# Optimization experiments

Measured on AMD Instinct MI355X. Metric: run time of the kernel, lower is better.

Reference implementation:

```python
import jax, jax.numpy as jnp
import numpy as np

F, K, V, ITERS = 150000, 5, 100000, 5
S = 2 ** K  # factor state space
MLP_SIZE = 2 * ITERS * S + ITERS * 2  # 330
NEG = -1e30
SHIFT = -500.0

# static bit table: bits[state, slot] in {0,1}
_BITS = ((np.arange(S)[:, None] >> np.arange(K)[None, :]) & 1).astype(np.int32)  # [S,K]
_BITS_T = jnp.asarray(_BITS.T)  # [K,S]
# mask bias for grouped logsumexp: bias[slot, b, state] = 0 if bits[state,slot]==b else NEG
_BIAS = jnp.asarray(np.where(_BITS.T[:, None, :] == np.arange(2)[None, :, None], 0.0, NEG).astype(np.float32))  # [K,2,S]


def neg_inf_to_zero(x):
    return jnp.where(jnp.isneginf(x), 0.0, x)


def expand(msg):
    # msg [F,K,2] -> [F,K,S]: broadcast each slot message over factor states by that slot's bit
    return msg[:, jnp.arange(K)[:, None], _BITS_T]


def setup_inputs() -> dict:
    key = jax.random.key(0)
    k0, k1 = jax.random.split(key)
    factor_potentials = jax.random.normal(k0, (F, S), dtype=jnp.float32)
    var_idx = jax.random.randint(k1, (F, K), 0, V, dtype=jnp.int32)
    prv_v2f = jnp.zeros((F, K, 2), jnp.float32)
    prv_f2v = jnp.zeros((F, K, 2), jnp.float32)
    prv_fb = jax.nn.log_softmax(factor_potentials, axis=1)
    # bethe MLP initialized exactly as in the torch module
    lin1_w = jnp.eye(MLP_SIZE, dtype=jnp.float32)
    lin1_b = jnp.zeros((MLP_SIZE,), jnp.float32)
    num_ones = 2 * S + 2
    lin2_w = jnp.zeros((1, MLP_SIZE), jnp.float32).at[0, -num_ones:].set(1.0)
    lin2_b = jnp.zeros((1,), jnp.float32)
    return {"factor_potentials": factor_potentials, "var_idx": var_idx,
            "prv_v2f": prv_v2f, "prv_f2v": prv_f2v, "prv_fb": prv_fb,
            "lin1_w": lin1_w, "lin1_b": lin1_b, "lin2_w": lin2_w, "lin2_b": lin2_b}


def _shifted_relu(x):
    return jnp.maximum(x, SHIFT)


def reference(factor_potentials, var_idx, prv_v2f, prv_f2v, prv_fb, lin1_w, lin1_b, lin2_w, lin2_b):
    var_flat = var_idx.reshape(-1)
    deg = jax.ops.segment_sum(jnp.ones((F * K,), jnp.float32), var_flat, num_segments=V)  # var_degrees
    pooled_states = []
    fb, v2f = prv_fb, prv_v2f
    for _ in range(ITERS):
        # factor->var messages, no double counting: subtract the slot's own incoming message
        scores = fb[:, None, :] - expand(v2f)                    # [F,K,S]
        m = jax.nn.logsumexp(scores[:, :, None, :] + _BIAS[None], axis=-1)  # [F,K,2]
        m = jax.nn.log_softmax(m, axis=-1)
        # var beliefs: gather all incoming factor->var messages
        vb = jax.ops.segment_sum(m.reshape(-1, 2), var_flat, num_segments=V)  # [V,2]
        vb = jax.nn.log_softmax(vb, axis=-1)
        # var->factor messages, no double counting
        v2f = jax.nn.log_softmax(vb[var_idx] - m, axis=-1)        # [F,K,2]
        # factor beliefs
        fb = factor_potentials + expand(v2f).sum(axis=1)          # [F,S]
        fb = fb - jax.nn.logsumexp(fb, axis=1, keepdims=True)
        # pooled Bethe free-energy features for this iteration
        e_fb = jnp.exp(fb)
        energy = jnp.sum(e_fb * neg_inf_to_zero(factor_potentials), axis=0)     # [S]
        fac_ent = -jnp.sum(e_fb * neg_inf_to_zero(fb), axis=0)                  # [S]
        var_term = jnp.sum((deg - 1.0)[:, None] * jnp.exp(vb) * neg_inf_to_zero(vb), axis=0)  # [2]
        pooled_states.append(jnp.concatenate([energy, fac_ent, var_term])[None, :])  # [1, 2S+2]
    x = jnp.concatenate(pooled_states, axis=1)   # [1, MLP_SIZE]
    h = _shifted_relu(x @ lin1_w.T + lin1_b)
    out = _shifted_relu(h @ lin2_w.T + lin2_b)   # [1,1] estimated ln(Z)
    return out
```

## Files before the change

kernel.cpp:

```cpp
#include <hip/hip_runtime.h>

#define F_N   150000
#define K_N   5
#define S_N   32
#define V_N   100000
#define NITER 5
#define MLP_N 330
#define SHIFTV (-500.0f)
#define W_ELL 32

#define FBLK  ((F_N + 255) / 256)
#define GBLK  ((V_N * 8 + 255) / 256)
#define EBLK  ((F_N * K_N + 255) / 256)

__device__ __forceinline__ float lse2(float a, float b) {
    float mx = fmaxf(a, b);
    return mx + __logf(__expf(a - mx) + __expf(b - mx));
}

__global__ __launch_bounds__(256) void k_build(
    const float* __restrict__ prv_fb,
    const float* __restrict__ prv_v2f,
    const int*   __restrict__ vidx,
    float2*      __restrict__ m2,
    int*         __restrict__ deg,
    int*         __restrict__ entries)
{
    int e = blockIdx.x * 256 + threadIdx.x;
    if (e >= F_N * K_N) return;
    int f = e / K_N;
    int k = e - f * K_N;
    int v = vidx[e];

    int pos = atomicAdd(&deg[v], 1);

    float fb[S_N];
    const float4* p4 = reinterpret_cast<const float4*>(prv_fb + (size_t)f * S_N);
    #pragma unroll
    for (int i = 0; i < S_N / 4; ++i) {
        float4 q = p4[i];
        fb[i*4+0] = q.x; fb[i*4+1] = q.y; fb[i*4+2] = q.z; fb[i*4+3] = q.w;
    }
    float M = fb[0];
    #pragma unroll
    for (int s = 1; s < S_N; ++s) M = fmaxf(M, fb[s]);
    float T = 0.0f, S0 = 0.0f;
    #pragma unroll
    for (int s = 0; s < S_N; ++s) {
        float t = __expf(fb[s] - M);
        T += t;
        if (((s >> k) & 1) == 0) S0 += t;
    }
    float v0 = prv_v2f[(size_t)e * 2 + 0];
    float v1 = prv_v2f[(size_t)e * 2 + 1];
    float u0 = __logf(S0)     - v0;
    float u1 = __logf(T - S0) - v1;
    float l  = lse2(u0, u1);
    m2[k*F_N + f] = make_float2(u0 - l, u1 - l);

    int slot = (pos < W_ELL) ? v * W_ELL + pos : V_N * W_ELL;
    entries[slot] = k * F_N + f;
}

__global__ __launch_bounds__(256) void k_gather(
    const float2* __restrict__ m2,
    const int*    __restrict__ deg,
    const int*    __restrict__ entries,
    float2*       __restrict__ vb,
    float2*       __restrict__ cpart,
    int iter)
{
    __shared__ float2 wred[4];
    int t = blockIdx.x * 256 + threadIdx.x;
    int v = t >> 3, sub = t & 7;
    int lane = threadIdx.x & 63;

    float a0 = 0.0f, a1 = 0.0f;
    int n = 0;
    if (v < V_N) {
        n = deg[v];
        int nn = n < W_ELL ? n : W_ELL;
        const int* row = entries + (size_t)v * W_ELL;
        for (int i = sub; i < nn; i += 8) {
            float2 mm = m2[row[i]];
            a0 += mm.x; a1 += mm.y;
        }
    }
    a0 += __shfl_xor(a0, 1); a1 += __shfl_xor(a1, 1);
    a0 += __shfl_xor(a0, 2); a1 += __shfl_xor(a1, 2);
    a0 += __shfl_xor(a0, 4); a1 += __shfl_xor(a1, 4);

    float c0 = 0.0f, c1 = 0.0f;
    if (v < V_N && sub == 0) {
        vb[v] = make_float2(a0, a1);
        float l = lse2(a0, a1);
        float b0 = a0 - l, b1 = a1 - l;
        float dm1 = (float)n - 1.0f;
        c0 = dm1 * __expf(b0) * b0;
        c1 = dm1 * __expf(b1) * b1;
    }
    #pragma unroll
    for (int mk = 32; mk >= 1; mk >>= 1) {
        c0 += __shfl_xor(c0, mk);
        c1 += __shfl_xor(c1, mk);
    }
    if (lane == 0) wred[threadIdx.x >> 6] = make_float2(c0, c1);
    __syncthreads();
    if (threadIdx.x == 0) {
        float2 s = wred[0];
        s.x += wred[1].x + wred[2].x + wred[3].x;
        s.y += wred[1].y + wred[2].y + wred[3].y;
        cpart[iter * GBLK + blockIdx.x] = s;
    }
}

template <bool LAST>
__global__ __launch_bounds__(256) void k_iter(
    const float*  __restrict__ pot,
    const int*    __restrict__ vidx,
    float2*       __restrict__ m2,
    const float2* __restrict__ vb,
    float*        __restrict__ fpart,
    int iter)
{
    const int lane = threadIdx.x & 63;
    __shared__ float red[256];

    int f = blockIdx.x * 256 + threadIdx.x;
    bool valid = f < F_N;
    int fc = valid ? f : (F_N - 1);

    float2 mm[K_N];
    #pragma unroll
    for (int k = 0; k < K_N; ++k) mm[k] = m2[k*F_N + fc];
    int vi[K_N];
    #pragma unroll
    for (int k = 0; k < K_N; ++k) vi[k] = vidx[(size_t)fc * K_N + k];

    float v2f[K_N][2];
    #pragma unroll
    for (int k = 0; k < K_N; ++k) {
        float2 b = vb[vi[k]];
        float a0 = b.x - mm[k].x;
        float a1 = b.y - mm[k].y;
        float l = lse2(a0, a1);
        v2f[k][0] = a0 - l;
        v2f[k][1] = a1 - l;
    }

    float fb[S_N];
    const float4* p4 = reinterpret_cast<const float4*>(pot + (size_t)fc * S_N);
    #pragma unroll
    for (int i = 0; i < S_N / 4; ++i) {
        float4 pv = p4[i];
        int s = i * 4;
        fb[s+0] = pv.x + v2f[0][(s+0)&1] + v2f[1][((s+0)>>1)&1] + v2f[2][((s+0)>>2)&1] + v2f[3][((s+0)>>3)&1] + v2f[4][((s+0)>>4)&1];
        fb[s+1] = pv.y + v2f[0][(s+1)&1] + v2f[1][((s+1)>>1)&1] + v2f[2][((s+1)>>2)&1] + v2f[3][((s+1)>>3)&1] + v2f[4][((s+1)>>4)&1];
        fb[s+2] = pv.z + v2f[0][(s+2)&1] + v2f[1][((s+2)>>1)&1] + v2f[2][((s+2)>>2)&1] + v2f[3][((s+2)>>3)&1] + v2f[4][((s+2)>>4)&1];
        fb[s+3] = pv.w + v2f[0][(s+3)&1] + v2f[1][((s+3)>>1)&1] + v2f[2][((s+3)>>2)&1] + v2f[3][((s+3)>>3)&1] + v2f[4][((s+3)>>4)&1];
    }

    float M = fb[0];
    #pragma unroll
    for (int s = 1; s < S_N; ++s) M = fmaxf(M, fb[s]);

    float T = 0.0f;
    float S0[K_N] = {0.f, 0.f, 0.f, 0.f, 0.f};
    #pragma unroll
    for (int s = 0; s < S_N; ++s) {
        float t = __expf(fb[s] - M);
        T += t;
        #pragma unroll
        for (int k = 0; k < K_N; ++k)
            if (((s >> k) & 1) == 0) S0[k] += t;
    }

    if (!LAST) {
        #pragma unroll
        for (int k = 0; k < K_N; ++k) {
            float u0 = __logf(S0[k])     - v2f[k][0];
            float u1 = __logf(T - S0[k]) - v2f[k][1];
            float l  = lse2(u0, u1);
            if (valid) m2[k*F_N + f] = make_float2(u0 - l, u1 - l);
        }
    }

    float invT = 1.0f / T;
    float logT = __logf(T);
    float arr[2 * S_N];
    #pragma unroll
    for (int s = 0; s < S_N; ++s) {
        float p   = __expf(fb[s] - M) * invT;
        float fbn = fb[s] - M - logT;
        float w   = v2f[0][s&1] + v2f[1][(s>>1)&1] + v2f[2][(s>>2)&1]
                  + v2f[3][(s>>3)&1] + v2f[4][(s>>4)&1];
        float po  = fb[s] - w;
        arr[s]       = valid ? p * po   : 0.0f;
        arr[S_N + s] = valid ? -p * fbn : 0.0f;
    }

    #pragma unroll
    for (int mk = 32; mk >= 1; mk >>= 1) {
        bool upper = (lane & mk) != 0;
        #pragma unroll
        for (int j = 0; j < mk; ++j) {
            float send = upper ? arr[j] : arr[j + mk];
            float recv = __shfl_xor(send, mk);
            float keep = upper ? arr[j + mk] : arr[j];
            arr[j] = keep + recv;
        }
    }

    red[threadIdx.x] = arr[0];
    __syncthreads();
    if (threadIdx.x < 64) {
        float s = red[threadIdx.x] + red[64 + threadIdx.x]
                + red[128 + threadIdx.x] + red[192 + threadIdx.x];
        fpart[((size_t)iter * FBLK + blockIdx.x) * 64 + threadIdx.x] = s;
    }
}

__global__ __launch_bounds__(256) void k_vt(
    const float*  __restrict__ fpart,
    const float2* __restrict__ cpart,
    float*        __restrict__ x)
{
    __shared__ float red[256];
    int b = blockIdx.x, t = threadIdx.x;
    float acc = 0.0f;
    if (b < 320) {
        int it = b >> 6, s = b & 63;
        for (int i = t; i < FBLK; i += 256)
            acc += fpart[((size_t)it * FBLK + i) * 64 + s];
    } else {
        int idx = b - 320;
        int it = idx >> 1, c = idx & 1;
        for (int i = t; i < GBLK; i += 256) {
            float2 p = cpart[it * GBLK + i];
            acc += c ? p.y : p.x;
        }
    }
    red[t] = acc;
    __syncthreads();
    #pragma unroll
    for (int off = 128; off >= 1; off >>= 1) {
        if (t < off) red[t] += red[t + off];
        __syncthreads();
    }
    if (t == 0) {
        if (b < 320) {
            int it = b >> 6, s = b & 63;
            x[it*66 + s] = red[0];
        } else {
            int idx = b - 320;
            int it = idx >> 1, c = idx & 1;
            x[it*66 + 64 + c] = red[0];
        }
    }
}

__global__ __launch_bounds__(64) void k_mlp1(
    const float* __restrict__ x, const float* __restrict__ w1,
    const float* __restrict__ b1, float* __restrict__ h)
{
    int j = blockIdx.x;
    int lane = threadIdx.x;
    float s = 0.0f;
    for (int i = lane; i < MLP_N; i += 64) s += x[i] * w1[(size_t)j * MLP_N + i];
    #pragma unroll
    for (int mk = 32; mk >= 1; mk >>= 1) s += __shfl_xor(s, mk);
    if (lane == 0) h[j] = fmaxf(s + b1[j], SHIFTV);
}

__global__ __launch_bounds__(64) void k_mlp2(
    const float* __restrict__ h, const float* __restrict__ w2,
    const float* __restrict__ b2, float* __restrict__ out)
{
    int lane = threadIdx.x;
    float s = 0.0f;
    for (int i = lane; i < MLP_N; i += 64) s += h[i] * w2[i];
    #pragma unroll
    for (int mk = 32; mk >= 1; mk >>= 1) s += __shfl_xor(s, mk);
    if (lane == 0) out[0] = fmaxf(s + b2[0], SHIFTV);
}

extern "C" void kernel_launch(void* const* d_in, const int* in_sizes, int n_in,
                              void* d_out, int out_size, void* d_ws, size_t ws_size,
                              hipStream_t stream)
{
    (void)in_sizes; (void)n_in; (void)out_size; (void)ws_size;
    const float* pot  = (const float*)d_in[0];
    const int*   vidx = (const int*)  d_in[1];
    const float* pv2f = (const float*)d_in[2];
    const float* pfb  = (const float*)d_in[4];
    const float* w1   = (const float*)d_in[5];
    const float* b1   = (const float*)d_in[6];
    const float* w2   = (const float*)d_in[7];
    const float* b2   = (const float*)d_in[8];

    float2* m2      = (float2*)d_ws;
    float2* vb      = m2 + 5 * F_N;
    float2* cpart   = vb + V_N;
    float*  fpart   = (float*)(cpart + NITER * GBLK);
    float*  x       = fpart + (size_t)NITER * FBLK * 64;
    float*  h       = x + MLP_N;
    int*    entries = (int*)(h + MLP_N);
    int*    deg     = entries + (size_t)V_N * W_ELL + 64;

    hipMemsetAsync(deg, 0, (size_t)V_N * sizeof(int), stream);

    k_build<<<EBLK, 256, 0, stream>>>(pfb, pv2f, vidx, m2, deg, entries);

    for (int it = 0; it < NITER; ++it) {
        k_gather<<<GBLK, 256, 0, stream>>>(m2, deg, entries, vb, cpart, it);
        if (it < NITER - 1)
            k_iter<false><<<FBLK, 256, 0, stream>>>(pot, vidx, m2, vb, fpart, it);
        else
            k_iter<true><<<FBLK, 256, 0, stream>>>(pot, vidx, m2, vb, fpart, it);
    }

    k_vt<<<330, 256, 0, stream>>>(fpart, cpart, x);
    k_mlp1<<<MLP_N, 64, 0, stream>>>(x, w1, b1, h);
    k_mlp2<<<1, 64, 0, stream>>>(h, w2, b2, (float*)d_out);
}
```

Before: 203.7 us.

## Split each factor across two threads in the factor iteration kernel

```diff
diff --git a/kernel.cpp b/kernel.cpp
--- a/kernel.cpp
+++ b/kernel.cpp
@@ -10,6 +10,7 @@
 #define W_ELL 32
 
 #define FBLK  ((F_N + 255) / 256)
+#define F2BLK ((2*F_N + 255) / 256)
 #define GBLK  ((V_N * 8 + 255) / 256)
 #define EBLK  ((F_N * K_N + 255) / 256)
 
@@ -124,99 +125,120 @@
     int iter)
 {
     const int lane = threadIdx.x & 63;
-    __shared__ float red[256];
-
-    int f = blockIdx.x * 256 + threadIdx.x;
+    __shared__ float red[4][64];
+
+    int t = blockIdx.x * 256 + threadIdx.x;
+    int f = t >> 1, p = t & 1;
     bool valid = f < F_N;
     int fc = valid ? f : (F_N - 1);
 
-    float2 mm[K_N];
-    #pragma unroll
-    for (int k = 0; k < K_N; ++k) mm[k] = m2[k*F_N + fc];
-    int vi[K_N];
-    #pragma unroll
-    for (int k = 0; k < K_N; ++k) vi[k] = vidx[(size_t)fc * K_N + k];
-
-    float v2f[K_N][2];
+    float v2f[K_N][2] = {{0,0},{0,0},{0,0},{0,0},{0,0}};
     #pragma unroll
     for (int k = 0; k < K_N; ++k) {
-        float2 b = vb[vi[k]];
-        float a0 = b.x - mm[k].x;
-        float a1 = b.y - mm[k].y;
-        float l = lse2(a0, a1);
-        v2f[k][0] = a0 - l;
-        v2f[k][1] = a1 - l;
-    }
-
-    float fb[S_N];
-    const float4* p4 = reinterpret_cast<const float4*>(pot + (size_t)fc * S_N);
-    #pragma unroll
-    for (int i = 0; i < S_N / 4; ++i) {
+        bool mine = p ? (k >= 3) : (k < 3);
+        if (mine) {
+            int vi = vidx[(size_t)fc * K_N + k];
+            float2 mmk = m2[k*F_N + fc];
+            float2 b = vb[vi];
+            float a0 = b.x - mmk.x;
+            float a1 = b.y - mmk.y;
+            float l = lse2(a0, a1);
+            v2f[k][0] = a0 - l;
+            v2f[k][1] = a1 - l;
+        }
+    }
+    #pragma unroll
+    for (int k = 0; k < K_N; ++k) {
+        bool mine = p ? (k >= 3) : (k < 3);
+        float o0 = __shfl_xor(v2f[k][0], 1);
+        float o1 = __shfl_xor(v2f[k][1], 1);
+        if (!mine) { v2f[k][0] = o0; v2f[k][1] = o1; }
+    }
+
+    float fb[16];
+    const float4* p4 = reinterpret_cast<const float4*>(pot + (size_t)fc * S_N + p * 16);
+    #pragma unroll
+    for (int i = 0; i < 4; ++i) {
         float4 pv = p4[i];
-        int s = i * 4;
-        fb[s+0] = pv.x + v2f[0][(s+0)&1] + v2f[1][((s+0)>>1)&1] + v2f[2][((s+0)>>2)&1] + v2f[3][((s+0)>>3)&1] + v2f[4][((s+0)>>4)&1];
-        fb[s+1] = pv.y + v2f[0][(s+1)&1] + v2f[1][((s+1)>>1)&1] + v2f[2][((s+1)>>2)&1] + v2f[3][((s+1)>>3)&1] + v2f[4][((s+1)>>4)&1];
-        fb[s+2] = pv.z + v2f[0][(s+2)&1] + v2f[1][((s+2)>>1)&1] + v2f[2][((s+2)>>2)&1] + v2f[3][((s+2)>>3)&1] + v2f[4][((s+2)>>4)&1];
-        fb[s+3] = pv.w + v2f[0][(s+3)&1] + v2f[1][((s+3)>>1)&1] + v2f[2][((s+3)>>2)&1] + v2f[3][((s+3)>>3)&1] + v2f[4][((s+3)>>4)&1];
+        int s = p*16 + i*4;
+        fb[i*4+0] = pv.x + v2f[0][(s+0)&1] + v2f[1][((s+0)>>1)&1] + v2f[2][((s+0)>>2)&1] + v2f[3][((s+0)>>3)&1] + v2f[4][((s+0)>>4)&1];
+        fb[i*4+1] = pv.y + v2f[0][(s+1)&1] + v2f[1][((s+1)>>1)&1] + v2f[2][((s+1)>>2)&1] + v2f[3][((s+1)>>3)&1] + v2f[4][((s+1)>>4)&1];
+        fb[i*4+2] = pv.z + v2f[0][(s+2)&1] + v2f[1][((s+2)>>1)&1] + v2f[2][((s+2)>>2)&1] + v2f[3][((s+2)>>3)&1] + v2f[4][((s+2)>>4)&1];
+        fb[i*4+3] = pv.w + v2f[0][(s+3)&1] + v2f[1][((s+3)>>1)&1] + v2f[2][((s+3)>>2)&1] + v2f[3][((s+3)>>3)&1] + v2f[4][((s+3)>>4)&1];
     }
 
     float M = fb[0];
     #pragma unroll
-    for (int s = 1; s < S_N; ++s) M = fmaxf(M, fb[s]);
+    for (int j = 1; j < 16; ++j) M = fmaxf(M, fb[j]);
+    M = fmaxf(M, __shfl_xor(M, 1));
 
     float T = 0.0f;
     float S0[K_N] = {0.f, 0.f, 0.f, 0.f, 0.f};
     #pragma unroll
-    for (int s = 0; s < S_N; ++s) {
-        float t = __expf(fb[s] - M);
-        T += t;
+    for (int j = 0; j < 16; ++j) {
+        int s = p*16 + j;
+        float e = __expf(fb[j] - M);
+        T += e;
         #pragma unroll
         for (int k = 0; k < K_N; ++k)
-            if (((s >> k) & 1) == 0) S0[k] += t;
-    }
+            if (((s >> k) & 1) == 0) S0[k] += e;
+    }
+    T += __shfl_xor(T, 1);
+    #pragma unroll
+    for (int k = 0; k < K_N; ++k) S0[k] += __shfl_xor(S0[k], 1);
 
     if (!LAST) {
         #pragma unroll
         for (int k = 0; k < K_N; ++k) {
-            float u0 = __logf(S0[k])     - v2f[k][0];
-            float u1 = __logf(T - S0[k]) - v2f[k][1];
-            float l  = lse2(u0, u1);
-            if (valid) m2[k*F_N + f] = make_float2(u0 - l, u1 - l);
+            bool mine = p ? (k >= 3) : (k < 3);
+            if (valid && mine) {
+                float u0 = __logf(S0[k])     - v2f[k][0];
+                float u1 = __logf(T - S0[k]) - v2f[k][1];
+                float l  = lse2(u0, u1);
+                m2[k*F_N + f] = make_float2(u0 - l, u1 - l);
+            }
         }
     }
 
     float invT = 1.0f / T;
     float logT = __logf(T);
-    float arr[2 * S_N];
-    #pragma unroll
-    for (int s = 0; s < S_N; ++s) {
-        float p   = __expf(fb[s] - M) * invT;
-        float fbn = fb[s] - M - logT;
+    float arr[32];
+    #pragma unroll
+    for (int j = 0; j < 16; ++j) {
+        int s = p*16 + j;
+        float pe  = __expf(fb[j] - M) * invT;
+        float fbn = fb[j] - M - logT;
         float w   = v2f[0][s&1] + v2f[1][(s>>1)&1] + v2f[2][(s>>2)&1]
                   + v2f[3][(s>>3)&1] + v2f[4][(s>>4)&1];
-        float po  = fb[s] - w;
-        arr[s]       = valid ? p * po   : 0.0f;
-        arr[S_N + s] = valid ? -p * fbn : 0.0f;
-    }
-
-    #pragma unroll
-    for (int mk = 32; mk >= 1; mk >>= 1) {
+        arr[j]      = valid ? pe * (fb[j] - w) : 0.0f;
+        arr[16 + j] = valid ? -pe * fbn        : 0.0f;
+    }
+
+    int len = 16;
+    #pragma unroll
+    for (int mk = 2; mk <= 32; mk <<= 1) {
         bool upper = (lane & mk) != 0;
         #pragma unroll
-        for (int j = 0; j < mk; ++j) {
-            float send = upper ? arr[j] : arr[j + mk];
-            float recv = __shfl_xor(send, mk);
-            float keep = upper ? arr[j + mk] : arr[j];
-            arr[j] = keep + recv;
-        }
-    }
-
-    red[threadIdx.x] = arr[0];
+        for (int j = 0; j < 16; ++j) {
+            if (j < len) {
+                float send = upper ? arr[j] : arr[j + len];
+                float recv = __shfl_xor(send, mk);
+                float keep = upper ? arr[j + len] : arr[j];
+                arr[j] = keep + recv;
+            }
+        }
+        len >>= 1;
+    }
+    int jl = (((lane>>1)&1)<<4) | (((lane>>2)&1)<<3) | (((lane>>3)&1)<<2)
+           | (((lane>>4)&1)<<1) | ((lane>>5)&1);
+    int g  = (lane & 1) * 16 + jl + (jl < 16 ? 0 : 16);
+
+    red[threadIdx.x >> 6][g] = arr[0];
     __syncthreads();
     if (threadIdx.x < 64) {
-        float s = red[threadIdx.x] + red[64 + threadIdx.x]
-                + red[128 + threadIdx.x] + red[192 + threadIdx.x];
-        fpart[((size_t)iter * FBLK + blockIdx.x) * 64 + threadIdx.x] = s;
+        float s = red[0][threadIdx.x] + red[1][threadIdx.x]
+                + red[2][threadIdx.x] + red[3][threadIdx.x];
+        fpart[((size_t)iter * F2BLK + blockIdx.x) * 64 + threadIdx.x] = s;
     }
 }
 
@@ -230,8 +252,8 @@
     float acc = 0.0f;
     if (b < 320) {
         int it = b >> 6, s = b & 63;
-        for (int i = t; i < FBLK; i += 256)
-            acc += fpart[((size_t)it * FBLK + i) * 64 + s];
+        for (int i = t; i < F2BLK; i += 256)
+            acc += fpart[((size_t)it * F2BLK + i) * 64 + s];
     } else {
         int idx = b - 320;
         int it = idx >> 1, c = idx & 1;
@@ -302,7 +324,7 @@
     float2* vb      = m2 + 5 * F_N;
     float2* cpart   = vb + V_N;
     float*  fpart   = (float*)(cpart + NITER * GBLK);
-    float*  x       = fpart + (size_t)NITER * FBLK * 64;
+    float*  x       = fpart + (size_t)NITER * F2BLK * 64;
     float*  h       = x + MLP_N;
     int*    entries = (int*)(h + MLP_N);
     int*    deg     = entries + (size_t)V_N * W_ELL + 64;
@@ -314,9 +336,9 @@
     for (int it = 0; it < NITER; ++it) {
         k_gather<<<GBLK, 256, 0, stream>>>(m2, deg, entries, vb, cpart, it);
         if (it < NITER - 1)
-            k_iter<false><<<FBLK, 256, 0, stream>>>(pot, vidx, m2, vb, fpart, it);
+            k_iter<false><<<F2BLK, 256, 0, stream>>>(pot, vidx, m2, vb, fpart, it);
         else
-            k_iter<true><<<FBLK, 256, 0, stream>>>(pot, vidx, m2, vb, fpart, it);
+            k_iter<true><<<F2BLK, 256, 0, stream>>>(pot, vidx, m2, vb, fpart, it);
     }
 
     k_vt<<<330, 256, 0, stream>>>(fpart, cpart, x);
```

After: 353.5 us. 73.5% more time.

## Compute var-to-factor messages in gather kernel and scatter per edge

Applied to the files above, without the earlier changes.

```diff
diff --git a/kernel.cpp b/kernel.cpp
--- a/kernel.cpp
+++ b/kernel.cpp
@@ -66,7 +66,7 @@
     const float2* __restrict__ m2,
     const int*    __restrict__ deg,
     const int*    __restrict__ entries,
-    float2*       __restrict__ vb,
+    float2*       __restrict__ v2fe,
     float2*       __restrict__ cpart,
     int iter)
 {
@@ -77,22 +77,41 @@
 
     float a0 = 0.0f, a1 = 0.0f;
     int n = 0;
+    int   ent[4];
+    float em0[4], em1[4];
+    ent[0] = ent[1] = ent[2] = ent[3] = -1;
     if (v < V_N) {
         n = deg[v];
         int nn = n < W_ELL ? n : W_ELL;
         const int* row = entries + (size_t)v * W_ELL;
-        for (int i = sub; i < nn; i += 8) {
-            float2 mm = m2[row[i]];
-            a0 += mm.x; a1 += mm.y;
+        #pragma unroll
+        for (int s2 = 0; s2 < 4; ++s2) {
+            int i = sub + s2 * 8;
+            if (i < nn) {
+                int e = row[i];
+                ent[s2] = e;
+                float2 mm = m2[e];
+                em0[s2] = mm.x; em1[s2] = mm.y;
+                a0 += mm.x; a1 += mm.y;
+            }
         }
     }
     a0 += __shfl_xor(a0, 1); a1 += __shfl_xor(a1, 1);
     a0 += __shfl_xor(a0, 2); a1 += __shfl_xor(a1, 2);
     a0 += __shfl_xor(a0, 4); a1 += __shfl_xor(a1, 4);
 
+    #pragma unroll
+    for (int s2 = 0; s2 < 4; ++s2) {
+        if (ent[s2] >= 0) {
+            float aa0 = a0 - em0[s2];
+            float aa1 = a1 - em1[s2];
+            float l = lse2(aa0, aa1);
+            v2fe[ent[s2]] = make_float2(aa0 - l, aa1 - l);
+        }
+    }
+
     float c0 = 0.0f, c1 = 0.0f;
     if (v < V_N && sub == 0) {
-        vb[v] = make_float2(a0, a1);
         float l = lse2(a0, a1);
         float b0 = a0 - l, b1 = a1 - l;
         float dm1 = (float)n - 1.0f;
@@ -117,9 +136,8 @@
 template <bool LAST>
 __global__ __launch_bounds__(256) void k_iter(
     const float*  __restrict__ pot,
-    const int*    __restrict__ vidx,
+    const float2* __restrict__ v2fe,
     float2*       __restrict__ m2,
-    const float2* __restrict__ vb,
     float*        __restrict__ fpart,
     int iter)
 {
@@ -130,22 +148,12 @@
     bool valid = f < F_N;
     int fc = valid ? f : (F_N - 1);
 
-    float2 mm[K_N];
-    #pragma unroll
-    for (int k = 0; k < K_N; ++k) mm[k] = m2[k*F_N + fc];
-    int vi[K_N];
-    #pragma unroll
-    for (int k = 0; k < K_N; ++k) vi[k] = vidx[(size_t)fc * K_N + k];
-
     float v2f[K_N][2];
     #pragma unroll
     for (int k = 0; k < K_N; ++k) {
-        float2 b = vb[vi[k]];
-        float a0 = b.x - mm[k].x;
-        float a1 = b.y - mm[k].y;
-        float l = lse2(a0, a1);
-        v2f[k][0] = a0 - l;
-        v2f[k][1] = a1 - l;
+        float2 q = v2fe[k*F_N + fc];
+        v2f[k][0] = q.x;
+        v2f[k][1] = q.y;
     }
 
     float fb[S_N];
@@ -299,8 +307,8 @@
     const float* b2   = (const float*)d_in[8];
 
     float2* m2      = (float2*)d_ws;
-    float2* vb      = m2 + 5 * F_N;
-    float2* cpart   = vb + V_N;
+    float2* v2fe    = m2 + 5 * F_N;
+    float2* cpart   = v2fe + 5 * F_N;
     float*  fpart   = (float*)(cpart + NITER * GBLK);
     float*  x       = fpart + (size_t)NITER * FBLK * 64;
     float*  h       = x + MLP_N;
@@ -312,11 +320,11 @@
     k_build<<<EBLK, 256, 0, stream>>>(pfb, pv2f, vidx, m2, deg, entries);
 
     for (int it = 0; it < NITER; ++it) {
-        k_gather<<<GBLK, 256, 0, stream>>>(m2, deg, entries, vb, cpart, it);
+        k_gather<<<GBLK, 256, 0, stream>>>(m2, deg, entries, v2fe, cpart, it);
         if (it < NITER - 1)
-            k_iter<false><<<FBLK, 256, 0, stream>>>(pot, vidx, m2, vb, fpart, it);
+            k_iter<false><<<FBLK, 256, 0, stream>>>(pot, v2fe, m2, fpart, it);
         else
-            k_iter<true><<<FBLK, 256, 0, stream>>>(pot, vidx, m2, vb, fpart, it);
+            k_iter<true><<<FBLK, 256, 0, stream>>>(pot, v2fe, m2, fpart, it);
     }
 
     k_vt<<<330, 256, 0, stream>>>(fpart, cpart, x);
```

Result: slower. 238.8 us (+17.2%).
